# Performance work log

Measured on AMD Instinct MI355X. Metric: run time of the kernel, lower is better.

Reference implementation:

```python
import jax, jax.numpy as jnp
import numpy as np

T, SEQ, IN, H, L, NC = 64, 128, 256, 512, 2, 10


def _xavier(key, shape):
    fan_out, fan_in = shape[0], shape[1]
    a = jnp.sqrt(6.0 / (fan_in + fan_out)).astype(jnp.float32)
    return jax.random.uniform(key, shape, jnp.float32, -a, a)


def setup_inputs() -> dict:
    key = jax.random.key(0)
    ks = jax.random.split(key, 16)
    inp = {"x": jax.random.normal(ks[0], (T, SEQ, IN), jnp.float32)}
    # LSTM layer 0 (input IN), layer 1 (input H). PyTorch gate order: i, f, g, o
    inp["w_ih0"] = _xavier(ks[1], (4 * H, IN))
    inp["w_hh0"] = _xavier(ks[2], (4 * H, H))
    inp["b_ih0"] = jnp.zeros((4 * H,), jnp.float32)
    inp["b_hh0"] = jnp.zeros((4 * H,), jnp.float32)
    inp["w_ih1"] = _xavier(ks[3], (4 * H, H))
    inp["w_hh1"] = _xavier(ks[4], (4 * H, H))
    inp["b_ih1"] = jnp.zeros((4 * H,), jnp.float32)
    inp["b_hh1"] = jnp.zeros((4 * H,), jnp.float32)
    # out_linear: Linear(SEQ*H, H) -> ReLU -> Linear(H, NC)
    inp["w1"] = _xavier(ks[5], (H, SEQ * H))
    inp["b1"] = jnp.zeros((H,), jnp.float32)
    inp["w2"] = _xavier(ks[6], (NC, H))
    inp["b2"] = jnp.zeros((NC,), jnp.float32)
    return inp


def _lstm_layer(x, w_ih, w_hh, b_ih, b_hh):
    # x: [T, B, I]; returns hidden sequence [T, B, H]
    B = x.shape[1]
    Hh = w_hh.shape[1]
    # precompute input-to-gate contributions for all timesteps
    xg = jnp.einsum('tbi,gi->tbg', x, w_ih) + b_ih  # [T, B, 4H]

    def step(carry, xg_t):
        h, c = carry
        g = xg_t + h @ w_hh.T + b_hh  # [B, 4H]
        i, f, gg, o = jnp.split(g, 4, axis=-1)
        i = jax.nn.sigmoid(i)
        f = jax.nn.sigmoid(f)
        gg = jnp.tanh(gg)
        o = jax.nn.sigmoid(o)
        c = f * c + i * gg
        h = o * jnp.tanh(c)
        return (h, c), h

    init = (jnp.zeros((B, Hh), x.dtype), jnp.zeros((B, Hh), x.dtype))
    _, ys = jax.lax.scan(step, init, xg)
    return ys


def reference(x, w_ih0, w_hh0, b_ih0, b_hh0, w_ih1, w_hh1, b_ih1, b_hh1, w1, b1, w2, b2):
    out = _lstm_layer(x, w_ih0, w_hh0, b_ih0, b_hh0)
    out = _lstm_layer(out, w_ih1, w_hh1, b_ih1, b_hh1)  # [T, SEQ, H]
    # dropout p=0.0 -> identity
    flat = out.reshape(out.shape[0], -1)  # [T, SEQ*H] (batched version of per-i loop)
    hmid = jax.nn.relu(flat @ w1.T + b1)
    return hmid @ w2.T + b2  # [T, NC]
```

## Files before the change

kernel.cpp:

```cpp
#include <hip/hip_runtime.h>

#define TT 64
#define BB 128
#define IND 256
#define HH 512
#define GG 2048
#define NCC 10
#define KFLAT 65536
#define HP2 520
#define SP 36

typedef __attribute__((ext_vector_type(8))) short bf16x8;
typedef __attribute__((ext_vector_type(4))) float floatx4;

__device__ __forceinline__ unsigned short f2bf(float x) {
    unsigned u = __builtin_bit_cast(unsigned, x);
    u += 0x7fffu + ((u >> 16) & 1u);
    return (unsigned short)(u >> 16);
}
__device__ __forceinline__ float bf2f(unsigned short h) {
    unsigned u = ((unsigned)h) << 16;
    return __builtin_bit_cast(float, u);
}
__device__ __forceinline__ float pk2f(unsigned u) {
    float hi = __builtin_bit_cast(float, u & 0xffff0000u);
    float lo = __builtin_bit_cast(float, u << 16);
    return hi + lo;
}

__global__ __launch_bounds__(256) void pack_split_kernel(
    const float* __restrict__ src, unsigned* __restrict__ dst, int n)
{
    for (int i = blockIdx.x * 256 + threadIdx.x; i < n; i += gridDim.x * 256) {
        float f = src[i];
        unsigned short hb = f2bf(f);
        unsigned short lb = f2bf(f - bf2f(hb));
        dst[i] = ((unsigned)hb << 16) | lb;
    }
}

__global__ __launch_bounds__(256) void gemm_pk_mfma(
    const unsigned* __restrict__ A, const unsigned* __restrict__ W,
    const float* __restrict__ b0, const float* __restrict__ b1,
    float* __restrict__ C, int K, int N)
{
    __shared__ short Ahi[128][SP], Alo[128][SP], Whi[128][SP], Wlo[128][SP];

    const int tid  = threadIdx.x;
    const int lane = tid & 63;
    const int wv   = tid >> 6;
    const int wm   = (wv & 1) * 64;
    const int wn   = (wv >> 1) * 64;
    const int l15  = lane & 15;
    const int quad = lane >> 4;
    const int m0   = blockIdx.x * 128;
    const int n0   = blockIdx.y * 128;

    floatx4 acc[4][4];
    #pragma unroll
    for (int i = 0; i < 4; ++i)
        #pragma unroll
        for (int j = 0; j < 4; ++j)
            acc[i][j] = (floatx4){0.f, 0.f, 0.f, 0.f};

    for (int kc = 0; kc < K; kc += 32) {
        #pragma unroll
        for (int it = 0; it < 4; ++it) {
            const int lin = it * 256 + tid;
            const int row = lin >> 3;
            const int c4  = (lin & 7) * 4;
            uint4 va = *(const uint4*)&A[(size_t)(m0 + row) * K + kc + c4];
            uint2 ah, al;
            ah.x = (va.x >> 16) | (va.y & 0xffff0000u);
            ah.y = (va.z >> 16) | (va.w & 0xffff0000u);
            al.x = (va.x & 0xffffu) | (va.y << 16);
            al.y = (va.z & 0xffffu) | (va.w << 16);
            *(uint2*)&Ahi[row][c4] = ah;
            *(uint2*)&Alo[row][c4] = al;
            uint4 vw = *(const uint4*)&W[(size_t)(n0 + row) * K + kc + c4];
            uint2 wh, wl;
            wh.x = (vw.x >> 16) | (vw.y & 0xffff0000u);
            wh.y = (vw.z >> 16) | (vw.w & 0xffff0000u);
            wl.x = (vw.x & 0xffffu) | (vw.y << 16);
            wl.y = (vw.z & 0xffffu) | (vw.w << 16);
            *(uint2*)&Whi[row][c4] = wh;
            *(uint2*)&Wlo[row][c4] = wl;
        }
        __syncthreads();

        bf16x8 afh[4], afl[4], bfh[4], bfl[4];
        #pragma unroll
        for (int i = 0; i < 4; ++i) {
            afh[i] = *(const bf16x8*)&Ahi[wm + i * 16 + l15][quad * 8];
            afl[i] = *(const bf16x8*)&Alo[wm + i * 16 + l15][quad * 8];
            bfh[i] = *(const bf16x8*)&Whi[wn + i * 16 + l15][quad * 8];
            bfl[i] = *(const bf16x8*)&Wlo[wn + i * 16 + l15][quad * 8];
        }
        #pragma unroll
        for (int i = 0; i < 4; ++i)
            #pragma unroll
            for (int j = 0; j < 4; ++j) {
                acc[i][j] = __builtin_amdgcn_mfma_f32_16x16x32_bf16(afh[i], bfh[j], acc[i][j], 0, 0, 0);
                acc[i][j] = __builtin_amdgcn_mfma_f32_16x16x32_bf16(afh[i], bfl[j], acc[i][j], 0, 0, 0);
                acc[i][j] = __builtin_amdgcn_mfma_f32_16x16x32_bf16(afl[i], bfh[j], acc[i][j], 0, 0, 0);
            }
        __syncthreads();
    }

    #pragma unroll
    for (int i = 0; i < 4; ++i) {
        #pragma unroll
        for (int j = 0; j < 4; ++j) {
            const int n = n0 + wn + j * 16 + l15;
            const float bias = b0[n] + b1[n];
            #pragma unroll
            for (int r = 0; r < 4; ++r) {
                const int m = m0 + wm + i * 16 + quad * 4 + r;
                C[(size_t)m * N + n] = acc[i][j][r] + bias;
            }
        }
    }
}

__device__ __forceinline__ unsigned stage8_atomic(
    const unsigned long long* __restrict__ src, int bb, int kk, unsigned exp,
    short (*Hs_hi)[HP2], short (*Hs_lo)[HP2])
{
    unsigned long long q0 = __hip_atomic_load(src + 0, __ATOMIC_RELAXED, __HIP_MEMORY_SCOPE_AGENT);
    unsigned long long q1 = __hip_atomic_load(src + 1, __ATOMIC_RELAXED, __HIP_MEMORY_SCOPE_AGENT);
    unsigned long long q2 = __hip_atomic_load(src + 2, __ATOMIC_RELAXED, __HIP_MEMORY_SCOPE_AGENT);
    unsigned long long q3 = __hip_atomic_load(src + 3, __ATOMIC_RELAXED, __HIP_MEMORY_SCOPE_AGENT);
    unsigned c0 = (unsigned)q0, c1 = (unsigned)(q0 >> 32);
    unsigned c2 = (unsigned)q1, c3 = (unsigned)(q1 >> 32);
    unsigned c4 = (unsigned)q2, c5 = (unsigned)(q2 >> 32);
    unsigned c6 = (unsigned)q3, c7 = (unsigned)(q3 >> 32);
    unsigned bad = ((c0 ^ exp) | (c1 ^ exp) | (c2 ^ exp) | (c3 ^ exp)
                  | (c4 ^ exp) | (c5 ^ exp) | (c6 ^ exp) | (c7 ^ exp)) & 0xFu;
    uint4 hiv, lov;
    hiv.x = (c0 >> 16) | (c1 & 0xffff0000u);
    hiv.y = (c2 >> 16) | (c3 & 0xffff0000u);
    hiv.z = (c4 >> 16) | (c5 & 0xffff0000u);
    hiv.w = (c6 >> 16) | (c7 & 0xffff0000u);
    lov.x = (c0 & 0xFFF0u) | ((c1 & 0xFFF0u) << 16);
    lov.y = (c2 & 0xFFF0u) | ((c3 & 0xFFF0u) << 16);
    lov.z = (c4 & 0xFFF0u) | ((c5 & 0xFFF0u) << 16);
    lov.w = (c6 & 0xFFF0u) | ((c7 & 0xFFF0u) << 16);
    *(uint4*)&Hs_hi[bb][kk] = hiv;
    *(uint4*)&Hs_lo[bb][kk] = lov;
    return bad;
}

__device__ __forceinline__ unsigned stage8_plain(
    const unsigned* __restrict__ src, int bb, int kk, unsigned exp,
    short (*Hs_hi)[HP2], short (*Hs_lo)[HP2])
{
    const uint4 v0 = *(const uint4*)(src);
    const uint4 v1 = *(const uint4*)(src + 4);
    unsigned bad = ((v0.x ^ exp) | (v0.y ^ exp) | (v0.z ^ exp) | (v0.w ^ exp)
                  | (v1.x ^ exp) | (v1.y ^ exp) | (v1.z ^ exp) | (v1.w ^ exp)) & 0xFu;
    uint4 hiv, lov;
    hiv.x = (v0.x >> 16) | (v0.y & 0xffff0000u);
    hiv.y = (v0.z >> 16) | (v0.w & 0xffff0000u);
    hiv.z = (v1.x >> 16) | (v1.y & 0xffff0000u);
    hiv.w = (v1.z >> 16) | (v1.w & 0xffff0000u);
    lov.x = (v0.x & 0xFFF0u) | ((v0.y & 0xFFF0u) << 16);
    lov.y = (v0.z & 0xFFF0u) | ((v0.w & 0xFFF0u) << 16);
    lov.z = (v1.x & 0xFFF0u) | ((v1.y & 0xFFF0u) << 16);
    lov.w = (v1.z & 0xFFF0u) | ((v1.w & 0xFFF0u) << 16);
    *(uint4*)&Hs_hi[bb][kk] = hiv;
    *(uint4*)&Hs_lo[bb][kk] = lov;
    return bad;
}

__device__ __forceinline__ void spin_flag(const unsigned* p) {
    while (__hip_atomic_load(p, __ATOMIC_RELAXED, __HIP_MEMORY_SCOPE_AGENT) == 0u) { }
}

__global__ __launch_bounds__(256, 1) void lstm_fused(
    const float* __restrict__ xg,
    const float* __restrict__ w_hh0,
    const float* __restrict__ w_ih1,
    const float* __restrict__ w_hh1,
    const float* __restrict__ b_ih1, const float* __restrict__ b_hh1,
    unsigned* __restrict__ hpack0,
    unsigned* __restrict__ hpack1,
    unsigned* __restrict__ flags)
{
    __shared__ short Ra_hi[32][HP2], Ra_lo[32][HP2];
    __shared__ short Xa_hi[32][HP2], Xa_lo[32][HP2];
    __shared__ float Gs[64][33];

    const int tid  = threadIdx.x;
    const int lane = tid & 63;
    const int wv   = tid >> 6;
    const bool isB = blockIdx.x >= 128;
    const int blk  = blockIdx.x & 127;
    const int bt   = blk & 3;
    const int jsl  = blk >> 2;
    const int j0   = jsl * 16;
    const int l15  = lane & 15;
    const int quad = lane >> 4;

    bf16x8 wa_hi[16], wa_lo[16], wx_hi[16], wx_lo[16];
    {
        const float* wsrc = isB ? w_hh1 : w_hh0;
        const float* wrow = wsrc + (size_t)(wv * HH + j0 + l15) * HH + quad * 8;
        #pragma unroll
        for (int kc = 0; kc < 16; ++kc) {
            float f[8];
            *(float4*)&f[0] = *(const float4*)&wrow[kc * 32];
            *(float4*)&f[4] = *(const float4*)&wrow[kc * 32 + 4];
            bf16x8 vh, vl;
            #pragma unroll
            for (int j = 0; j < 8; ++j) {
                unsigned short hb = f2bf(f[j]);
                vh[j] = (short)hb;
                vl[j] = (short)f2bf(f[j] - bf2f(hb));
            }
            wa_hi[kc] = vh; wa_lo[kc] = vl;
        }
        if (isB) {
            const float* xrow = w_ih1 + (size_t)(wv * HH + j0 + l15) * HH + quad * 8;
            #pragma unroll
            for (int kc = 0; kc < 16; ++kc) {
                float f[8];
                *(float4*)&f[0] = *(const float4*)&xrow[kc * 32];
                *(float4*)&f[4] = *(const float4*)&xrow[kc * 32 + 4];
                bf16x8 vh, vl;
                #pragma unroll
                for (int j = 0; j < 8; ++j) {
                    unsigned short hb = f2bf(f[j]);
                    vh[j] = (short)hb;
                    vl[j] = (short)f2bf(f[j] - bf2f(hb));
                }
                wx_hi[kc] = vh; wx_lo[kc] = vl;
            }
        }
    }

    const int j_u = tid & 15;
    const int bu  = tid >> 4;
    float bias_i = 0.f, bias_f = 0.f, bias_g = 0.f, bias_o = 0.f;
    if (isB) {
        bias_i = b_ih1[j0 + j_u]            + b_hh1[j0 + j_u];
        bias_f = b_ih1[HH + j0 + j_u]       + b_hh1[HH + j0 + j_u];
        bias_g = b_ih1[2 * HH + j0 + j_u]   + b_hh1[2 * HH + j0 + j_u];
        bias_o = b_ih1[3 * HH + j0 + j_u]   + b_hh1[3 * HH + j0 + j_u];
    }

    unsigned* hp_rec = isB ? hpack1 : hpack0;
    const int layerBase = isB ? 65 : 0;
    float c0 = 0.f, c1 = 0.f;

    for (int t = 0; t < TT; ++t) {
        const unsigned* rec_base = hp_rec + (size_t)t * (BB * HH) + (size_t)bt * 32 * HH;
        const unsigned* inp_base = hpack0 + (size_t)(t + 1) * (BB * HH) + (size_t)bt * 32 * HH;
        const unsigned expR = (unsigned)t % 9u;
        const unsigned expX = (unsigned)(t + 1) % 9u;

        float xgv[2][4];
        if (!isB) {
            #pragma unroll
            for (int ccell = 0; ccell < 2; ++ccell) {
                const int b = bu + ccell * 16;
                const float* base = xg + (size_t)t * (BB * GG)
                                  + (size_t)(bt * 32 + b) * GG + j0 + j_u;
                xgv[ccell][0] = base[0];
                xgv[ccell][1] = base[HH];
                xgv[ccell][2] = base[2 * HH];
                xgv[ccell][3] = base[3 * HH];
            }
        }

        const unsigned* fR = flags + ((layerBase + t) * 4 + bt) * 32;
        const unsigned* fX = flags + ((t + 1) * 4 + bt) * 32;
        if (lane < 32) {
            if (t > 0 && lane != jsl) spin_flag(fR + lane);
        } else if (isB) {
            spin_flag(fX + (lane - 32));
        }
        asm volatile("" ::: "memory");

        unsigned missR = 0, missX = 0;
        #pragma unroll
        for (int p = 0; p < 8; ++p) {
            const int idx = p * 2048 + tid * 8;
            unsigned bad = stage8_plain(rec_base + idx, idx >> 9, idx & 511,
                                        expR, Ra_hi, Ra_lo);
            missR |= (bad ? 1u : 0u) << p;
        }
        if (isB) {
            #pragma unroll
            for (int p = 0; p < 8; ++p) {
                const int idx = p * 2048 + tid * 8;
                unsigned bad = stage8_plain(inp_base + idx, idx >> 9, idx & 511,
                                            expX, Xa_hi, Xa_lo);
                missX |= (bad ? 1u : 0u) << p;
            }
        }
        while (missR | missX) {
            #pragma unroll
            for (int p = 0; p < 8; ++p) {
                if (missR & (1u << p)) {
                    const int idx = p * 2048 + tid * 8;
                    if (!stage8_atomic((const unsigned long long*)(rec_base + idx),
                                       idx >> 9, idx & 511, expR, Ra_hi, Ra_lo))
                        missR &= ~(1u << p);
                }
                if (missX & (1u << p)) {
                    const int idx = p * 2048 + tid * 8;
                    if (!stage8_atomic((const unsigned long long*)(inp_base + idx),
                                       idx >> 9, idx & 511, expX, Xa_hi, Xa_lo))
                        missX &= ~(1u << p);
                }
            }
        }
        __syncthreads();

        floatx4 aR0 = {0.f,0.f,0.f,0.f}, aR1 = {0.f,0.f,0.f,0.f};
        floatx4 aX0 = {0.f,0.f,0.f,0.f}, aX1 = {0.f,0.f,0.f,0.f};
        #pragma unroll
        for (int kc = 0; kc < 16; ++kc) {
            const int off = kc * 32 + quad * 8;
            bf16x8 r0h = *(const bf16x8*)&Ra_hi[l15][off];
            bf16x8 r0l = *(const bf16x8*)&Ra_lo[l15][off];
            bf16x8 r1h = *(const bf16x8*)&Ra_hi[16 + l15][off];
            bf16x8 r1l = *(const bf16x8*)&Ra_lo[16 + l15][off];
            aR0 = __builtin_amdgcn_mfma_f32_16x16x32_bf16(wa_hi[kc], r0h, aR0, 0, 0, 0);
            aR1 = __builtin_amdgcn_mfma_f32_16x16x32_bf16(wa_hi[kc], r1h, aR1, 0, 0, 0);
            aR0 = __builtin_amdgcn_mfma_f32_16x16x32_bf16(wa_hi[kc], r0l, aR0, 0, 0, 0);
            aR1 = __builtin_amdgcn_mfma_f32_16x16x32_bf16(wa_hi[kc], r1l, aR1, 0, 0, 0);
            aR0 = __builtin_amdgcn_mfma_f32_16x16x32_bf16(wa_lo[kc], r0h, aR0, 0, 0, 0);
            aR1 = __builtin_amdgcn_mfma_f32_16x16x32_bf16(wa_lo[kc], r1h, aR1, 0, 0, 0);
            if (isB) {
                bf16x8 x0h = *(const bf16x8*)&Xa_hi[l15][off];
                bf16x8 x0l = *(const bf16x8*)&Xa_lo[l15][off];
                bf16x8 x1h = *(const bf16x8*)&Xa_hi[16 + l15][off];
                bf16x8 x1l = *(const bf16x8*)&Xa_lo[16 + l15][off];
                aX0 = __builtin_amdgcn_mfma_f32_16x16x32_bf16(wx_hi[kc], x0h, aX0, 0, 0, 0);
                aX1 = __builtin_amdgcn_mfma_f32_16x16x32_bf16(wx_hi[kc], x1h, aX1, 0, 0, 0);
                aX0 = __builtin_amdgcn_mfma_f32_16x16x32_bf16(wx_hi[kc], x0l, aX0, 0, 0, 0);
                aX1 = __builtin_amdgcn_mfma_f32_16x16x32_bf16(wx_hi[kc], x1l, aX1, 0, 0, 0);
                aX0 = __builtin_amdgcn_mfma_f32_16x16x32_bf16(wx_lo[kc], x0h, aX0, 0, 0, 0);
                aX1 = __builtin_amdgcn_mfma_f32_16x16x32_bf16(wx_lo[kc], x1h, aX1, 0, 0, 0);
            }
        }

        #pragma unroll
        for (int r = 0; r < 4; ++r) {
            Gs[wv * 16 + quad * 4 + r][l15]      = aR0[r] + aX0[r];
            Gs[wv * 16 + quad * 4 + r][16 + l15] = aR1[r] + aX1[r];
        }
        __syncthreads();

        const unsigned tag = (unsigned)(t + 1) % 9u;
        #pragma unroll
        for (int ccell = 0; ccell < 2; ++ccell) {
            const int b = bu + ccell * 16;
            float gi = Gs[j_u][b],      gf = Gs[16 + j_u][b];
            float gg = Gs[32 + j_u][b], go = Gs[48 + j_u][b];
            if (isB) { gi += bias_i; gf += bias_f; gg += bias_g; go += bias_o; }
            else     { gi += xgv[ccell][0]; gf += xgv[ccell][1];
                       gg += xgv[ccell][2]; go += xgv[ccell][3]; }
            const float si = 1.f / (1.f + __expf(-gi));
            const float sf = 1.f / (1.f + __expf(-gf));
            const float tg = 2.f / (1.f + __expf(-2.f * gg)) - 1.f;
            const float so = 1.f / (1.f + __expf(-go));
            float& cr = ccell ? c1 : c0;
            cr = sf * cr + si * tg;
            const float th = 2.f / (1.f + __expf(-2.f * cr)) - 1.f;
            const float hval = so * th;
            const unsigned short hb = f2bf(hval);
            const unsigned short lb = f2bf(hval - bf2f(hb));
            const unsigned pk = ((unsigned)hb << 16) | ((unsigned)lb & 0xFFF0u) | tag;
            __hip_atomic_store(
                &hp_rec[(size_t)(t + 1) * (BB * HH) + (size_t)(bt * 32 + b) * HH + j0 + j_u],
                pk, __ATOMIC_RELAXED, __HIP_MEMORY_SCOPE_AGENT);
        }
        __syncthreads();

        if (tid == 0)
            __hip_atomic_store(
                flags + ((layerBase + (t + 1)) * 4 + bt) * 32 + jsl,
                1u, __ATOMIC_RELAXED, __HIP_MEMORY_SCOPE_AGENT);
    }
}

__global__ __launch_bounds__(256) void cls_partial_kernel(
    const unsigned* __restrict__ A, const float* __restrict__ W,
    float* __restrict__ part)
{
    const int n0 = blockIdx.x * 64;
    const int s  = blockIdx.y;
    const int kbase = s * 2048;
    const int tid = threadIdx.x;
    __shared__ float As[32][68];
    __shared__ float Bs[32][68];
    const int tm = tid >> 4, tn = tid & 15;
    float acc[4][4] = {};

    for (int kt = 0; kt < 2048; kt += 32) {
        #pragma unroll
        for (int q = tid; q < 512; q += 256) {
            const int mm = q >> 3;
            const int kq = q & 7;
            uint4 v = *(const uint4*)&A[(size_t)mm * KFLAT + kbase + kt + kq * 4];
            As[kq*4+0][mm] = pk2f(v.x & 0xFFFFFFF0u); As[kq*4+1][mm] = pk2f(v.y & 0xFFFFFFF0u);
            As[kq*4+2][mm] = pk2f(v.z & 0xFFFFFFF0u); As[kq*4+3][mm] = pk2f(v.w & 0xFFFFFFF0u);
            float4 w = *(const float4*)&W[(size_t)(n0 + mm) * KFLAT + kbase + kt + kq * 4];
            Bs[kq*4+0][mm] = w.x; Bs[kq*4+1][mm] = w.y;
            Bs[kq*4+2][mm] = w.z; Bs[kq*4+3][mm] = w.w;
        }
        __syncthreads();
        #pragma unroll
        for (int k = 0; k < 32; ++k) {
            float4 a = *(const float4*)&As[k][tm * 4];
            float4 b = *(const float4*)&Bs[k][tn * 4];
            acc[0][0] += a.x*b.x; acc[0][1] += a.x*b.y; acc[0][2] += a.x*b.z; acc[0][3] += a.x*b.w;
            acc[1][0] += a.y*b.x; acc[1][1] += a.y*b.y; acc[1][2] += a.y*b.z; acc[1][3] += a.y*b.w;
            acc[2][0] += a.z*b.x; acc[2][1] += a.z*b.y; acc[2][2] += a.z*b.z; acc[2][3] += a.z*b.w;
            acc[3][0] += a.w*b.x; acc[3][1] += a.w*b.y; acc[3][2] += a.w*b.z; acc[3][3] += a.w*b.w;
        }
        __syncthreads();
    }
    #pragma unroll
    for (int i = 0; i < 4; ++i) {
        const int m = tm * 4 + i;
        #pragma unroll
        for (int j = 0; j < 4; ++j) {
            part[((size_t)s * 64 + m) * 512 + n0 + tn * 4 + j] = acc[i][j];
        }
    }
}

__global__ __launch_bounds__(256) void cls_final_kernel(
    const float* __restrict__ part, const float* __restrict__ b1,
    const float* __restrict__ w2, const float* __restrict__ b2,
    float* __restrict__ out)
{
    const int t = blockIdx.x;
    __shared__ float hm[512];
    for (int n = threadIdx.x; n < 512; n += 256) {
        float sacc = b1[n];
        for (int sl = 0; sl < 32; ++sl)
            sacc += part[((size_t)sl * 64 + t) * 512 + n];
        hm[n] = fmaxf(sacc, 0.f);
    }
    __syncthreads();
    if (threadIdx.x < NCC) {
        float sacc = b2[threadIdx.x];
        const float* wr = w2 + (size_t)threadIdx.x * 512;
        for (int n = 0; n < 512; ++n) sacc += hm[n] * wr[n];
        out[t * NCC + threadIdx.x] = sacc;
    }
}

extern "C" void kernel_launch(void* const* d_in, const int* in_sizes, int n_in,
                              void* d_out, int out_size, void* d_ws, size_t ws_size,
                              hipStream_t stream)
{
    const float* x     = (const float*)d_in[0];
    const float* w_ih0 = (const float*)d_in[1];
    const float* w_hh0 = (const float*)d_in[2];
    const float* b_ih0 = (const float*)d_in[3];
    const float* b_hh0 = (const float*)d_in[4];
    const float* w_ih1 = (const float*)d_in[5];
    const float* w_hh1 = (const float*)d_in[6];
    const float* b_ih1 = (const float*)d_in[7];
    const float* b_hh1 = (const float*)d_in[8];
    const float* w1    = (const float*)d_in[9];
    const float* b1    = (const float*)d_in[10];
    const float* w2    = (const float*)d_in[11];
    const float* b2    = (const float*)d_in[12];
    float* out = (float*)d_out;

    float*    ws     = (float*)d_ws;
    float*    xg     = ws;
    unsigned* hpack0 = (unsigned*)(xg + (size_t)8192 * 2048);
    unsigned* hpack1 = hpack0 + (size_t)65 * BB * HH;
    unsigned* xpk    = hpack1;
    unsigned* w0pk   = xpk + (size_t)8192 * IND;
    float*    part   = (float*)(hpack1 + (size_t)65 * BB * HH);
    unsigned* flags  = (unsigned*)part;

    pack_split_kernel<<<1024, 256, 0, stream>>>(x, xpk, 8192 * IND);
    pack_split_kernel<<<512,  256, 0, stream>>>(w_ih0, w0pk, GG * IND);
    hipMemsetAsync(hpack0, 0, (size_t)BB * HH * sizeof(unsigned), stream);
    hipMemsetAsync(flags, 0, (size_t)2 * 65 * 4 * 32 * sizeof(unsigned), stream);

    gemm_pk_mfma<<<dim3(8192 / 128, GG / 128), 256, 0, stream>>>(
        xpk, w0pk, b_ih0, b_hh0, xg, IND, GG);

    hipMemsetAsync(hpack1, 0, (size_t)BB * HH * sizeof(unsigned), stream);

    lstm_fused<<<256, 256, 0, stream>>>(
        xg, w_hh0, w_ih1, w_hh1, b_ih1, b_hh1, hpack0, hpack1, flags);

    cls_partial_kernel<<<dim3(512 / 64, 32), 256, 0, stream>>>(
        hpack1 + (size_t)BB * HH, w1, part);
    cls_final_kernel<<<64, 256, 0, stream>>>(part, b1, w2, b2, out);
}
```

Measured before the change: 987.8 us.

## Compute layer-1 input projection before waiting on recurrent hidden state

Layer-1 blocks now wait only for the layer-0 output flag, stage that tile and run its input-projection MFMAs, and only then wait on their own recurrent flags and stage the recurrent tile. The input-side work moves off the recurrent critical path, so it overlaps with the wait for other blocks' previous-step hidden state. Flag spinning moves to wave 0 and is followed by a block barrier, which adds extra __syncthreads per step. The two partial accumulators are merged into one.

Measured after the change: 912.5 us. -7.6%, faster.

```diff
diff --git a/kernel.cpp b/kernel.cpp
--- a/kernel.cpp
+++ b/kernel.cpp
@@ -172,6 +172,31 @@
     return bad;
 }
 
+__device__ __forceinline__ void stage_tile(
+    const unsigned* __restrict__ base, unsigned exp, int tid,
+    short (*Hs_hi)[HP2], short (*Hs_lo)[HP2])
+{
+    unsigned miss = 0;
+    #pragma unroll
+    for (int p = 0; p < 8; ++p) {
+        const int idx = p * 2048 + tid * 8;
+        unsigned bad = stage8_plain(base + idx, idx >> 9, idx & 511,
+                                    exp, Hs_hi, Hs_lo);
+        miss |= (bad ? 1u : 0u) << p;
+    }
+    while (miss) {
+        #pragma unroll
+        for (int p = 0; p < 8; ++p) {
+            if (miss & (1u << p)) {
+                const int idx = p * 2048 + tid * 8;
+                if (!stage8_atomic((const unsigned long long*)(base + idx),
+                                   idx >> 9, idx & 511, exp, Hs_hi, Hs_lo))
+                    miss &= ~(1u << p);
+            }
+        }
+    }
+}
+
 __device__ __forceinline__ void spin_flag(const unsigned* p) {
     while (__hip_atomic_load(p, __ATOMIC_RELAXED, __HIP_MEMORY_SCOPE_AGENT) == 0u) { }
 }
@@ -257,9 +282,36 @@
         const unsigned* inp_base = hpack0 + (size_t)(t + 1) * (BB * HH) + (size_t)bt * 32 * HH;
         const unsigned expR = (unsigned)t % 9u;
         const unsigned expX = (unsigned)(t + 1) % 9u;
-
+        const unsigned* fR = flags + ((layerBase + t) * 4 + bt) * 32;
+        const unsigned* fX = flags + ((t + 1) * 4 + bt) * 32;
+
+        floatx4 a0 = {0.f,0.f,0.f,0.f}, a1 = {0.f,0.f,0.f,0.f};
         float xgv[2][4];
-        if (!isB) {
+
+        if (isB) {
+            if (wv == 0 && lane < 32) spin_flag(fX + lane);
+            __syncthreads();
+            stage_tile(inp_base, expX, tid, Xa_hi, Xa_lo);
+            __syncthreads();
+            #pragma unroll
+            for (int kc = 0; kc < 16; ++kc) {
+                const int off = kc * 32 + quad * 8;
+                bf16x8 x0h = *(const bf16x8*)&Xa_hi[l15][off];
+                bf16x8 x0l = *(const bf16x8*)&Xa_lo[l15][off];
+                bf16x8 x1h = *(const bf16x8*)&Xa_hi[16 + l15][off];
+                bf16x8 x1l = *(const bf16x8*)&Xa_lo[16 + l15][off];
+                a0 = __builtin_amdgcn_mfma_f32_16x16x32_bf16(wx_hi[kc], x0h, a0, 0, 0, 0);
+                a1 = __builtin_amdgcn_mfma_f32_16x16x32_bf16(wx_hi[kc], x1h, a1, 0, 0, 0);
+                a0 = __builtin_amdgcn_mfma_f32_16x16x32_bf16(wx_hi[kc], x0l, a0, 0, 0, 0);
+                a1 = __builtin_amdgcn_mfma_f32_16x16x32_bf16(wx_hi[kc], x1l, a1, 0, 0, 0);
+                a0 = __builtin_amdgcn_mfma_f32_16x16x32_bf16(wx_lo[kc], x0h, a0, 0, 0, 0);
+                a1 = __builtin_amdgcn_mfma_f32_16x16x32_bf16(wx_lo[kc], x1h, a1, 0, 0, 0);
+            }
+            if (wv == 0 && lane < 32 && t > 0 && lane != jsl) spin_flag(fR + lane);
+            __syncthreads();
+            stage_tile(rec_base, expR, tid, Ra_hi, Ra_lo);
+            __syncthreads();
+        } else {
             #pragma unroll
             for (int ccell = 0; ccell < 2; ++ccell) {
                 const int b = bu + ccell * 16;
@@ -270,55 +322,12 @@
                 xgv[ccell][2] = base[2 * HH];
                 xgv[ccell][3] = base[3 * HH];
             }
-        }
-
-        const unsigned* fR = flags + ((layerBase + t) * 4 + bt) * 32;
-        const unsigned* fX = flags + ((t + 1) * 4 + bt) * 32;
-        if (lane < 32) {
-            if (t > 0 && lane != jsl) spin_flag(fR + lane);
-        } else if (isB) {
-            spin_flag(fX + (lane - 32));
-        }
-        asm volatile("" ::: "memory");
-
-        unsigned missR = 0, missX = 0;
-        #pragma unroll
-        for (int p = 0; p < 8; ++p) {
-            const int idx = p * 2048 + tid * 8;
-            unsigned bad = stage8_plain(rec_base + idx, idx >> 9, idx & 511,
-                                        expR, Ra_hi, Ra_lo);
-            missR |= (bad ? 1u : 0u) << p;
-        }
-        if (isB) {
-            #pragma unroll
-            for (int p = 0; p < 8; ++p) {
-                const int idx = p * 2048 + tid * 8;
-                unsigned bad = stage8_plain(inp_base + idx, idx >> 9, idx & 511,
-                                            expX, Xa_hi, Xa_lo);
-                missX |= (bad ? 1u : 0u) << p;
-            }
-        }
-        while (missR | missX) {
-            #pragma unroll
-            for (int p = 0; p < 8; ++p) {
-                if (missR & (1u << p)) {
-                    const int idx = p * 2048 + tid * 8;
-                    if (!stage8_atomic((const unsigned long long*)(rec_base + idx),
-                                       idx >> 9, idx & 511, expR, Ra_hi, Ra_lo))
-                        missR &= ~(1u << p);
-                }
-                if (missX & (1u << p)) {
-                    const int idx = p * 2048 + tid * 8;
-                    if (!stage8_atomic((const unsigned long long*)(inp_base + idx),
-                                       idx >> 9, idx & 511, expX, Xa_hi, Xa_lo))
-                        missX &= ~(1u << p);
-                }
-            }
-        }
-        __syncthreads();
-
-        floatx4 aR0 = {0.f,0.f,0.f,0.f}, aR1 = {0.f,0.f,0.f,0.f};
-        floatx4 aX0 = {0.f,0.f,0.f,0.f}, aX1 = {0.f,0.f,0.f,0.f};
+            if (wv == 0 && lane < 32 && t > 0 && lane != jsl) spin_flag(fR + lane);
+            __syncthreads();
+            stage_tile(rec_base, expR, tid, Ra_hi, Ra_lo);
+            __syncthreads();
+        }
+
         #pragma unroll
         for (int kc = 0; kc < 16; ++kc) {
             const int off = kc * 32 + quad * 8;
@@ -326,30 +335,18 @@
             bf16x8 r0l = *(const bf16x8*)&Ra_lo[l15][off];
             bf16x8 r1h = *(const bf16x8*)&Ra_hi[16 + l15][off];
             bf16x8 r1l = *(const bf16x8*)&Ra_lo[16 + l15][off];
-            aR0 = __builtin_amdgcn_mfma_f32_16x16x32_bf16(wa_hi[kc], r0h, aR0, 0, 0, 0);
-            aR1 = __builtin_amdgcn_mfma_f32_16x16x32_bf16(wa_hi[kc], r1h, aR1, 0, 0, 0);
-            aR0 = __builtin_amdgcn_mfma_f32_16x16x32_bf16(wa_hi[kc], r0l, aR0, 0, 0, 0);
-            aR1 = __builtin_amdgcn_mfma_f32_16x16x32_bf16(wa_hi[kc], r1l, aR1, 0, 0, 0);
-            aR0 = __builtin_amdgcn_mfma_f32_16x16x32_bf16(wa_lo[kc], r0h, aR0, 0, 0, 0);
-            aR1 = __builtin_amdgcn_mfma_f32_16x16x32_bf16(wa_lo[kc], r1h, aR1, 0, 0, 0);
-            if (isB) {
-                bf16x8 x0h = *(const bf16x8*)&Xa_hi[l15][off];
-                bf16x8 x0l = *(const bf16x8*)&Xa_lo[l15][off];
-                bf16x8 x1h = *(const bf16x8*)&Xa_hi[16 + l15][off];
-                bf16x8 x1l = *(const bf16x8*)&Xa_lo[16 + l15][off];
-                aX0 = __builtin_amdgcn_mfma_f32_16x16x32_bf16(wx_hi[kc], x0h, aX0, 0, 0, 0);
-                aX1 = __builtin_amdgcn_mfma_f32_16x16x32_bf16(wx_hi[kc], x1h, aX1, 0, 0, 0);
-                aX0 = __builtin_amdgcn_mfma_f32_16x16x32_bf16(wx_hi[kc], x0l, aX0, 0, 0, 0);
-                aX1 = __builtin_amdgcn_mfma_f32_16x16x32_bf16(wx_hi[kc], x1l, aX1, 0, 0, 0);
-                aX0 = __builtin_amdgcn_mfma_f32_16x16x32_bf16(wx_lo[kc], x0h, aX0, 0, 0, 0);
-                aX1 = __builtin_amdgcn_mfma_f32_16x16x32_bf16(wx_lo[kc], x1h, aX1, 0, 0, 0);
-            }
+            a0 = __builtin_amdgcn_mfma_f32_16x16x32_bf16(wa_hi[kc], r0h, a0, 0, 0, 0);
+            a1 = __builtin_amdgcn_mfma_f32_16x16x32_bf16(wa_hi[kc], r1h, a1, 0, 0, 0);
+            a0 = __builtin_amdgcn_mfma_f32_16x16x32_bf16(wa_hi[kc], r0l, a0, 0, 0, 0);
+            a1 = __builtin_amdgcn_mfma_f32_16x16x32_bf16(wa_hi[kc], r1l, a1, 0, 0, 0);
+            a0 = __builtin_amdgcn_mfma_f32_16x16x32_bf16(wa_lo[kc], r0h, a0, 0, 0, 0);
+            a1 = __builtin_amdgcn_mfma_f32_16x16x32_bf16(wa_lo[kc], r1h, a1, 0, 0, 0);
         }
 
         #pragma unroll
         for (int r = 0; r < 4; ++r) {
-            Gs[wv * 16 + quad * 4 + r][l15]      = aR0[r] + aX0[r];
-            Gs[wv * 16 + quad * 4 + r][16 + l15] = aR1[r] + aX1[r];
+            Gs[wv * 16 + quad * 4 + r][l15]      = a0[r];
+            Gs[wv * 16 + quad * 4 + r][16 + l15] = a1[r];
         }
         __syncthreads();
 
```
